# Performance work log

Hardware: AMD Instinct MI355X
Metric: run time of the kernel (lower is better)

The kernel has to match this reference:

```python
import jax, jax.numpy as jnp
import numpy as np

B, N, C, H = 2, 2048, 1024, 16
D = C // H
NEG = -1e9  # keras Softmax large negative for masked positions


def setup_inputs() -> dict:
    key = jax.random.key(0)
    ks = jax.random.split(key, 10)
    s = lambda fan_in: 1.0 / np.sqrt(fan_in)
    return {
        "x": jax.random.normal(ks[0], (B, N, C), jnp.float32),
        "mask": jnp.ones((B, 1, 1, N), jnp.bool_),
        "Wqkv": jax.random.normal(ks[1], (C, 3 * C), jnp.float32) * s(C),
        "bqkv": jnp.zeros((3 * C,), jnp.float32),
        "Wl": jax.random.normal(ks[2], (H, H), jnp.float32) * s(H),
        "bl": jnp.zeros((H,), jnp.float32),
        "Ww": jax.random.normal(ks[3], (H, H), jnp.float32) * s(H),
        "bw": jnp.zeros((H,), jnp.float32),
        "Wp": jax.random.normal(ks[4], (C, C), jnp.float32) * s(C),
        "bp": jnp.zeros((C,), jnp.float32),
    }


def reference(x, mask, Wqkv, bqkv, Wl, bl, Ww, bw, Wp, bp):
    scale = jnp.asarray(D ** -0.5, x.dtype)
    qkv = x @ Wqkv + bqkv                                  # [B,N,3C]
    qkv = qkv.reshape(B, N, 3, H, D).transpose(2, 0, 3, 1, 4)  # [3,B,H,N,D]
    q, k, v = qkv[0] * scale, qkv[1], qkv[2]
    attn = jnp.einsum("bhnd,bhmd->bhnm", q, k)             # [B,H,N,N]
    # pre-softmax talking-heads: mix head axis
    attn = jnp.einsum("bhnm,hg->bgnm", attn, Wl) + bl[None, :, None, None]
    # keras Softmax with boolean mask: add -1e9 where mask is False
    attn = attn + (1.0 - mask.astype(attn.dtype)) * NEG
    attn = jax.nn.softmax(attn, axis=-1)
    # post-softmax talking-heads
    attn = jnp.einsum("bhnm,hg->bgnm", attn, Ww) + bw[None, :, None, None]
    out = jnp.einsum("bhnm,bhmd->bhnd", attn, v)           # [B,H,N,D]
    out = out.transpose(0, 2, 1, 3).reshape(B, N, C)
    return out @ Wp + bp
```

## Files before the change

kernel.cpp:

```cpp
#include <hip/hip_runtime.h>
#include <hip/hip_bf16.h>


typedef __bf16 bf16_t;
typedef __bf16 bf16x8 __attribute__((ext_vector_type(8)));
typedef float f32x4 __attribute__((ext_vector_type(4)));

#define DEV static __device__ __forceinline__

static constexpr float NEGV = -1e9f;

DEV f32x4 mfma16(bf16x8 a, bf16x8 b, f32x4 c) {
  return __builtin_amdgcn_mfma_f32_16x16x32_bf16(a, b, c, 0, 0, 0);
}

DEV bf16x8 zero8() {
  bf16x8 z;
#pragma unroll
  for (int j = 0; j < 8; ++j) z[j] = (bf16_t)0.0f;
  return z;
}

DEV uint32_t pkbf(float lo, float hi) {
  union { bf16_t f; unsigned short s; } a, b;
  a.f = (bf16_t)lo; b.f = (bf16_t)hi;
  return (uint32_t)a.s | ((uint32_t)b.s << 16);
}

union U84 { uint32_t u[4]; bf16x8 v; };

__global__ __launch_bounds__(256) void mask_prep(const unsigned char* __restrict__ raw,
                                                 unsigned char* __restrict__ canon,
                                                 unsigned char* __restrict__ allflag) {
  __shared__ int c0, c12, f0, f1;
  const int tid = threadIdx.x;
  if (tid == 0) { c0 = 0; c12 = 0; f0 = 1; f1 = 1; }
  __syncthreads();
  int l0 = 0, l12 = 0;
  for (int i = tid; i < 4096; i += 256) {
    unsigned char v = raw[i];
    if (v) {
      int r = i & 3;
      if (r == 0) l0++;
      else if (r < 3) l12++;
    }
  }
  if (l0) atomicAdd(&c0, l0);
  if (l12) atomicAdd(&c12, l12);
  __syncthreads();
  const int mode = (c0 == 0) ? 2 : ((c12 > 0) ? 0 : 1);
  for (int i = tid; i < 4096; i += 256) {
    bool t;
    if (mode == 0)      t = raw[i] != 0;
    else if (mode == 1) t = ((const int*)raw)[i] != 0;
    else                t = ((const float*)raw)[i] != 0.0f;
    canon[i] = t ? 1 : 0;
    if (!t) atomicAnd(i < 2048 ? &f0 : &f1, 0);
  }
  __syncthreads();
  if (tid == 0) { allflag[0] = (unsigned char)f0; allflag[1] = (unsigned char)f1; }
}

__global__ __launch_bounds__(256) void gemm_kernel(
    const float* __restrict__ Af, const bf16_t* __restrict__ Ab,
    const float* __restrict__ Bw, const float* __restrict__ bias,
    float* __restrict__ outf,
    bf16_t* __restrict__ Qs, bf16_t* __restrict__ Ks, bf16_t* __restrict__ Vt,
    int K, int Nn, int epi) {
  __shared__ bf16_t As[64][40];
  __shared__ bf16_t Bs[64][40];
  const int tid = threadIdx.x;
  const int lane = tid & 63, wid = tid >> 6;
  const int bx = blockIdx.x, by = blockIdx.y;
  const int wr = (wid >> 1) * 32, wc = (wid & 1) * 32;
  const int lr = lane & 15, kq = lane >> 4;

  f32x4 acc[2][2];
#pragma unroll
  for (int i = 0; i < 2; ++i)
#pragma unroll
    for (int j = 0; j < 2; ++j) acc[i][j] = (f32x4){0.f, 0.f, 0.f, 0.f};

  for (int kt = 0; kt < K; kt += 32) {
    {
      const int row = tid >> 2, c8 = (tid & 3) * 8;
      if (epi == 0) {
        const float* p = Af + (size_t)(bx * 64 + row) * K + kt + c8;
        float4 v0 = *(const float4*)p;
        float4 v1 = *(const float4*)(p + 4);
        bf16x8 v;
        v[0] = (bf16_t)v0.x; v[1] = (bf16_t)v0.y; v[2] = (bf16_t)v0.z; v[3] = (bf16_t)v0.w;
        v[4] = (bf16_t)v1.x; v[5] = (bf16_t)v1.y; v[6] = (bf16_t)v1.z; v[7] = (bf16_t)v1.w;
        *(bf16x8*)&As[row][c8] = v;
      } else {
        *(bf16x8*)&As[row][c8] =
            *(const bf16x8*)(Ab + (size_t)(bx * 64 + row) * K + kt + c8);
      }
      const int krow = tid >> 3, n8 = (tid & 7) * 8;
      const float* bp = Bw + (size_t)(kt + krow) * Nn + by * 64 + n8;
      float4 b0 = *(const float4*)bp;
      float4 b1 = *(const float4*)(bp + 4);
      Bs[n8 + 0][krow] = (bf16_t)b0.x; Bs[n8 + 1][krow] = (bf16_t)b0.y;
      Bs[n8 + 2][krow] = (bf16_t)b0.z; Bs[n8 + 3][krow] = (bf16_t)b0.w;
      Bs[n8 + 4][krow] = (bf16_t)b1.x; Bs[n8 + 5][krow] = (bf16_t)b1.y;
      Bs[n8 + 6][krow] = (bf16_t)b1.z; Bs[n8 + 7][krow] = (bf16_t)b1.w;
    }
    __syncthreads();
#pragma unroll
    for (int rt = 0; rt < 2; ++rt) {
      bf16x8 af = *(const bf16x8*)&As[wr + rt * 16 + lr][kq * 8];
#pragma unroll
      for (int ct = 0; ct < 2; ++ct) {
        bf16x8 bf = *(const bf16x8*)&Bs[wc + ct * 16 + lr][kq * 8];
        acc[rt][ct] = mfma16(af, bf, acc[rt][ct]);
      }
    }
    __syncthreads();
  }

#pragma unroll
  for (int rt = 0; rt < 2; ++rt)
#pragma unroll
    for (int ct = 0; ct < 2; ++ct)
#pragma unroll
      for (int r = 0; r < 4; ++r) {
        const int grow = bx * 64 + wr + rt * 16 + kq * 4 + r;
        const int gcol = by * 64 + wc + ct * 16 + lr;
        const float v = acc[rt][ct][r] + bias[gcol];
        if (epi == 0) {
          const int t = gcol >> 10, h = (gcol >> 6) & 15, d = gcol & 63;
          const int b = grow >> 11, n = grow & 2047;
          if (t == 0)
            Qs[(((size_t)b * 16 + h) * 2048 + n) * 64 + d] = (bf16_t)(v * 0.125f);
          else if (t == 1)
            Ks[(((size_t)b * 16 + h) * 2048 + n) * 64 + d] = (bf16_t)v;
          else
            Vt[(((size_t)b * 16 + h) * 64 + d) * 2048 + n] = (bf16_t)v;
        } else {
          outf[(size_t)grow * Nn + gcol] = v;
        }
      }
}

__global__ __launch_bounds__(256) void vsum_kernel(const bf16_t* __restrict__ Vt,
                                                   float* __restrict__ Vsum) {
  const int lane = threadIdx.x & 63, wid = threadIdx.x >> 6;
  const int row = blockIdx.x * 4 + wid;
  const bf16_t* p = Vt + (size_t)row * 2048;
  float s = 0.f;
#pragma unroll
  for (int it = 0; it < 4; ++it) {
    bf16x8 v = *(const bf16x8*)(p + it * 512 + lane * 8);
#pragma unroll
    for (int j = 0; j < 8; ++j) s += (float)v[j];
  }
#pragma unroll
  for (int off = 32; off; off >>= 1) s += __shfl_xor(s, off);
  if (lane == 0) Vsum[row] = s;
}

__global__ __launch_bounds__(512, 2) void attn_fused(
    const bf16_t* __restrict__ Qs, const bf16_t* __restrict__ Ks,
    const bf16_t* __restrict__ Vt, const unsigned char* __restrict__ canon,
    const unsigned char* __restrict__ allflag,
    const float* __restrict__ Wl, const float* __restrict__ bl,
    const float* __restrict__ Ww, const float* __restrict__ bw,
    const float* __restrict__ Vsum, bf16_t* __restrict__ AO) {
  __shared__ uint32_t Sb[512 * 10];
  __shared__ uint32_t Fb[16 * 324];
  const int tid = threadIdx.x, lane = tid & 63, wid = tid >> 6;
  const int c = lane & 15, kq = lane >> 4;
  const int id = blockIdx.x;
  const int b = (id >> 2) & 1;
  const int nt = ((id >> 3) << 2) | (id & 3);
  const int n0 = nt * 16;
  const int bh0 = b * 16 + 2 * wid;
  const bool allt = allflag[b] != 0;

  bf16x8 wlf, wwf;
#pragma unroll
  for (int j = 0; j < 8; ++j) {
    const int k = kq * 8 + j;
    wlf[j] = (k < 16) ? (bf16_t)Wl[k * 16 + c] : (bf16_t)0.0f;
    wwf[j] = (k < 16) ? (bf16_t)Ww[k * 16 + c] : (bf16_t)0.0f;
  }
  f32x4 blv;
#pragma unroll
  for (int r = 0; r < 4; ++r) blv[r] = bl[kq * 4 + r];

  bf16x8 qf[2][2];
#pragma unroll
  for (int hh = 0; hh < 2; ++hh)
#pragma unroll
    for (int ks = 0; ks < 2; ++ks)
      qf[hh][ks] = *(const bf16x8*)(Qs + ((size_t)(bh0 + hh) * 2048 + n0 + c) * 64 +
                                    ks * 32 + kq * 8);

  struct KF { bf16x8 f[2][2][2]; };
  auto loadK = [&](int v) {
    KF k;
    const int m0 = (v < 64 ? v : 63) * 32;
#pragma unroll
    for (int hh = 0; hh < 2; ++hh)
#pragma unroll
      for (int mt = 0; mt < 2; ++mt)
#pragma unroll
        for (int ks = 0; ks < 2; ++ks)
          k.f[hh][mt][ks] = *(const bf16x8*)(Ks + ((size_t)(bh0 + hh) * 2048 + m0 +
                                                   mt * 16 + c) * 64 + ks * 32 + kq * 8);
    return k;
  };

  auto stage = [&](const KF& k) {
#pragma unroll
    for (int mt = 0; mt < 2; ++mt) {
      f32x4 a0 = (f32x4){0.f, 0.f, 0.f, 0.f};
      f32x4 a1 = (f32x4){0.f, 0.f, 0.f, 0.f};
      a0 = mfma16(qf[0][0], k.f[0][mt][0], a0);
      a0 = mfma16(qf[0][1], k.f[0][mt][1], a0);
      a1 = mfma16(qf[1][0], k.f[1][mt][0], a1);
      a1 = mfma16(qf[1][1], k.f[1][mt][1], a1);
#pragma unroll
      for (int r = 0; r < 4; ++r) {
        const int p = (kq * 4 + r) * 32 + mt * 16 + c;
        Sb[p * 10 + (wid ^ (kq & 1))] = pkbf(a0[r], a1[r]);
      }
    }
  };

  auto gatherS = [&](int pp) {
    const int prow = (wid * 4 + pp) * 16 + c;
    const int bp = (prow >> 7) & 1;
    if (kq < 2) {
      U84 t;
#pragma unroll
      for (int i = 0; i < 4; ++i) t.u[i] = Sb[prow * 10 + ((kq * 4 + i) ^ bp)];
      return t.v;
    }
    return zero8();
  };

  float lacc[4][2];
#pragma unroll
  for (int r = 0; r < 4; ++r) { lacc[r][0] = 0.f; lacc[r][1] = 0.f; }
  {
    KF kf = loadK(0);
    for (int u = 0; u < 64; ++u) {
      stage(kf);
      kf = loadK(u + 1);
      __syncthreads();
#pragma unroll
      for (int pp = 0; pp < 4; ++pp) {
        bf16x8 sf = gatherS(pp);
        f32x4 d1 = mfma16(wlf, sf, blv);
        if (!allt && !canon[b * 2048 + u * 32 + (pp & 1) * 16 + c]) {
          d1[0] += NEGV; d1[1] += NEGV; d1[2] += NEGV; d1[3] += NEGV;
        }
        const int ns = pp >> 1;
#pragma unroll
        for (int r = 0; r < 4; ++r) lacc[r][ns] += __expf(d1[r]);
      }
      __syncthreads();
    }
  }
  float invl[4][2];
#pragma unroll
  for (int r = 0; r < 4; ++r)
#pragma unroll
    for (int ns = 0; ns < 2; ++ns) {
      float s = lacc[r][ns];
      s += __shfl_xor(s, 1);
      s += __shfl_xor(s, 2);
      s += __shfl_xor(s, 4);
      s += __shfl_xor(s, 8);
      invl[r][ns] = 1.0f / s;
    }

  f32x4 oacc[2][4];
#pragma unroll
  for (int i = 0; i < 2; ++i)
#pragma unroll
    for (int j = 0; j < 4; ++j) oacc[i][j] = (f32x4){0.f, 0.f, 0.f, 0.f};
  {
    KF kf = loadK(0);
    for (int u = 0; u < 64; ++u) {
      stage(kf);
      kf = loadK(u + 1);
      __syncthreads();
      bf16x8 vr[2][4];
#pragma unroll
      for (int g2h = 0; g2h < 2; ++g2h)
#pragma unroll
        for (int dt = 0; dt < 4; ++dt)
          vr[g2h][dt] = *(const bf16x8*)(Vt + ((size_t)(bh0 + g2h) * 64 + dt * 16 + c) *
                                                  2048 + u * 32 + kq * 8);
#pragma unroll
      for (int pp = 0; pp < 4; ++pp) {
        bf16x8 sf = gatherS(pp);
        f32x4 d1 = mfma16(wlf, sf, blv);
        if (!allt && !canon[b * 2048 + u * 32 + (pp & 1) * 16 + c]) {
          d1[0] += NEGV; d1[1] += NEGV; d1[2] += NEGV; d1[3] += NEGV;
        }
        const int ns = pp >> 1;
        const float e0 = __expf(d1[0]) * invl[0][ns];
        const float e1 = __expf(d1[1]) * invl[1][ns];
        const float e2 = __expf(d1[2]) * invl[2][ns];
        const float e3 = __expf(d1[3]) * invl[3][ns];
        const int prow = (wid * 4 + pp) * 16 + c;
        uint2 ew;
        ew.x = pkbf(e0, e1);
        ew.y = pkbf(e2, e3);
        *(uint2*)&Sb[prow * 10 + kq * 2] = ew;
      }
      asm volatile("s_waitcnt lgkmcnt(0)" ::: "memory");
      __builtin_amdgcn_sched_barrier(0);
#pragma unroll
      for (int pp = 0; pp < 4; ++pp) {
        const int pg = wid * 4 + pp;
        const int prow = pg * 16 + c;
        bf16x8 ef;
        if (kq < 2) {
          U84 t;
#pragma unroll
          for (int i = 0; i < 4; ++i) t.u[i] = Sb[prow * 10 + kq * 4 + i];
          ef = t.v;
        } else ef = zero8();
        f32x4 d2 = mfma16(wwf, ef, (f32x4){0.f, 0.f, 0.f, 0.f});
        const int nl = pg >> 1, ml = (pg & 1) * 16 + c;
        const int wm = (ml >> 1) ^ ((nl & 3) << 2);
#pragma unroll
        for (int r = 0; r < 4; ++r)
          ((bf16_t*)Fb)[(((kq * 4 + r) * 324) + nl * 20 + wm) * 2 + (ml & 1)] =
              (bf16_t)d2[r];
      }
      __syncthreads();
#pragma unroll
      for (int g2h = 0; g2h < 2; ++g2h) {
        bf16x8 af = *(const bf16x8*)&Fb[(2 * wid + g2h) * 324 + c * 20 +
                                        ((kq ^ (c & 3)) << 2)];
#pragma unroll
        for (int dt = 0; dt < 4; ++dt)
          oacc[g2h][dt] = mfma16(af, vr[g2h][dt], oacc[g2h][dt]);
      }
    }
  }

#pragma unroll
  for (int g2h = 0; g2h < 2; ++g2h) {
    const int g2 = 2 * wid + g2h;
    const float bwv = bw[g2];
#pragma unroll
    for (int dt = 0; dt < 4; ++dt) {
      const float vs = Vsum[(size_t)(b * 16 + g2) * 64 + dt * 16 + c];
#pragma unroll
      for (int r = 0; r < 4; ++r) {
        const int n = n0 + kq * 4 + r;
        AO[((size_t)b * 2048 + n) * 1024 + g2 * 64 + dt * 16 + c] =
            (bf16_t)(oacc[g2h][dt][r] + bwv * vs);
      }
    }
  }
}

extern "C" void kernel_launch(void* const* d_in, const int* in_sizes, int n_in,
                              void* d_out, int out_size, void* d_ws, size_t ws_size,
                              hipStream_t stream) {
  const float* x = (const float*)d_in[0];
  const unsigned char* mask = (const unsigned char*)d_in[1];
  const float* Wqkv = (const float*)d_in[2];
  const float* bqkv = (const float*)d_in[3];
  const float* Wl = (const float*)d_in[4];
  const float* bl = (const float*)d_in[5];
  const float* Ww = (const float*)d_in[6];
  const float* bw = (const float*)d_in[7];
  const float* Wp = (const float*)d_in[8];
  const float* bp = (const float*)d_in[9];
  float* out = (float*)d_out;

  char* w = (char*)d_ws;
  auto alloc = [&](size_t bytes) {
    char* p = w;
    w += (bytes + 255) & ~(size_t)255;
    return p;
  };
  bf16_t* Qs = (bf16_t*)alloc((size_t)2 * 16 * 2048 * 64 * 2);
  bf16_t* Ks = (bf16_t*)alloc((size_t)2 * 16 * 2048 * 64 * 2);
  bf16_t* Vt = (bf16_t*)alloc((size_t)2 * 16 * 2048 * 64 * 2);
  bf16_t* AO = (bf16_t*)alloc((size_t)4096 * 1024 * 2);
  float* Vsum = (float*)alloc((size_t)2048 * 4);
  unsigned char* canon = (unsigned char*)alloc(4096);
  unsigned char* allflag = (unsigned char*)alloc(256);

  mask_prep<<<dim3(1), dim3(256), 0, stream>>>(mask, canon, allflag);
  gemm_kernel<<<dim3(64, 48), dim3(256), 0, stream>>>(
      x, (const bf16_t*)nullptr, Wqkv, bqkv, nullptr, Qs, Ks, Vt, 1024, 3072, 0);
  vsum_kernel<<<dim3(512), dim3(256), 0, stream>>>(Vt, Vsum);
  attn_fused<<<dim3(256), dim3(512), 0, stream>>>(Qs, Ks, Vt, canon, allflag, Wl, bl,
                                                  Ww, bw, Vsum, AO);
  gemm_kernel<<<dim3(64, 16), dim3(256), 0, stream>>>(
      (const float*)nullptr, AO, Wp, bp, out, nullptr, nullptr, nullptr, 1024, 1024, 1);
}
```

Measured before the change: 567.4 us.

## Double-buffer attention stages, halve block size, shuffle-based post-softmax mixing

Restructures the fused talking-heads attention kernel to use 256-thread blocks with each wave handling four heads. Double-buffered score and mixed-probability LDS tiles let the next tile's QK^T staging and the previous tile's PV MFMAs overlap the current tile's softmax work. This removes one barrier per iteration and the LDS round trip for the post-softmax head mix, which now goes through cross-lane shuffles. In exchange it uses more registers per wave (four heads of accumulators) and more LDS for the second buffers.

```diff
diff --git a/kernel.cpp b/kernel.cpp
--- a/kernel.cpp
+++ b/kernel.cpp
@@ -159,22 +159,21 @@
   if (lane == 0) Vsum[row] = s;
 }
 
-__global__ __launch_bounds__(512, 2) void attn_fused(
+__global__ __launch_bounds__(256, 2) void attn_fused(
     const bf16_t* __restrict__ Qs, const bf16_t* __restrict__ Ks,
     const bf16_t* __restrict__ Vt, const unsigned char* __restrict__ canon,
     const unsigned char* __restrict__ allflag,
     const float* __restrict__ Wl, const float* __restrict__ bl,
     const float* __restrict__ Ww, const float* __restrict__ bw,
     const float* __restrict__ Vsum, bf16_t* __restrict__ AO) {
-  __shared__ uint32_t Sb[512 * 10];
-  __shared__ uint32_t Fb[16 * 324];
+  __shared__ uint32_t Sb[2][5120];
+  __shared__ uint32_t Fb[2][16 * 260];
   const int tid = threadIdx.x, lane = tid & 63, wid = tid >> 6;
   const int c = lane & 15, kq = lane >> 4;
   const int id = blockIdx.x;
-  const int b = (id >> 2) & 1;
-  const int nt = ((id >> 3) << 2) | (id & 3);
-  const int n0 = nt * 16;
-  const int bh0 = b * 16 + 2 * wid;
+  const int b = id & 1;
+  const int n0 = (id >> 1) * 16;
+  const int h0 = 4 * wid;
   const bool allt = allflag[b] != 0;
 
   bf16x8 wlf, wwf;
@@ -188,86 +187,85 @@
 #pragma unroll
   for (int r = 0; r < 4; ++r) blv[r] = bl[kq * 4 + r];
 
-  bf16x8 qf[2][2];
-#pragma unroll
-  for (int hh = 0; hh < 2; ++hh)
+  bf16x8 qf[4][2];
+#pragma unroll
+  for (int hh = 0; hh < 4; ++hh)
 #pragma unroll
     for (int ks = 0; ks < 2; ++ks)
-      qf[hh][ks] = *(const bf16x8*)(Qs + ((size_t)(bh0 + hh) * 2048 + n0 + c) * 64 +
-                                    ks * 32 + kq * 8);
-
-  struct KF { bf16x8 f[2][2][2]; };
-  auto loadK = [&](int v) {
-    KF k;
-    const int m0 = (v < 64 ? v : 63) * 32;
-#pragma unroll
-    for (int hh = 0; hh < 2; ++hh)
-#pragma unroll
-      for (int mt = 0; mt < 2; ++mt)
-#pragma unroll
-        for (int ks = 0; ks < 2; ++ks)
-          k.f[hh][mt][ks] = *(const bf16x8*)(Ks + ((size_t)(bh0 + hh) * 2048 + m0 +
-                                                   mt * 16 + c) * 64 + ks * 32 + kq * 8);
-    return k;
+      qf[hh][ks] = *(const bf16x8*)(Qs + ((size_t)(b * 16 + h0 + hh) * 2048 + n0 + c) *
+                                             64 + ks * 32 + kq * 8);
+
+  auto stage = [&](int v, uint32_t* sb) {
+#pragma unroll
+    for (int hp = 0; hp < 2; ++hp) {
+      bf16x8 kf[2][2][2];
+#pragma unroll
+      for (int h2 = 0; h2 < 2; ++h2)
+#pragma unroll
+        for (int mt = 0; mt < 2; ++mt)
+#pragma unroll
+          for (int ks = 0; ks < 2; ++ks)
+            kf[h2][mt][ks] =
+                *(const bf16x8*)(Ks + ((size_t)(b * 16 + h0 + hp * 2 + h2) * 2048 +
+                                       v * 32 + mt * 16 + c) * 64 + ks * 32 + kq * 8);
+#pragma unroll
+      for (int mt = 0; mt < 2; ++mt) {
+        f32x4 a0 = (f32x4){0.f, 0.f, 0.f, 0.f};
+        f32x4 a1 = (f32x4){0.f, 0.f, 0.f, 0.f};
+        a0 = mfma16(qf[hp * 2 + 0][0], kf[0][mt][0], a0);
+        a0 = mfma16(qf[hp * 2 + 0][1], kf[0][mt][1], a0);
+        a1 = mfma16(qf[hp * 2 + 1][0], kf[1][mt][0], a1);
+        a1 = mfma16(qf[hp * 2 + 1][1], kf[1][mt][1], a1);
+#pragma unroll
+        for (int r = 0; r < 4; ++r) {
+          const int p = (kq * 4 + r) * 32 + mt * 16 + c;
+          sb[p * 10 + ((2 * wid + hp) ^ (kq & 1))] = pkbf(a0[r], a1[r]);
+        }
+      }
+    }
   };
 
-  auto stage = [&](const KF& k) {
-#pragma unroll
-    for (int mt = 0; mt < 2; ++mt) {
-      f32x4 a0 = (f32x4){0.f, 0.f, 0.f, 0.f};
-      f32x4 a1 = (f32x4){0.f, 0.f, 0.f, 0.f};
-      a0 = mfma16(qf[0][0], k.f[0][mt][0], a0);
-      a0 = mfma16(qf[0][1], k.f[0][mt][1], a0);
-      a1 = mfma16(qf[1][0], k.f[1][mt][0], a1);
-      a1 = mfma16(qf[1][1], k.f[1][mt][1], a1);
-#pragma unroll
-      for (int r = 0; r < 4; ++r) {
-        const int p = (kq * 4 + r) * 32 + mt * 16 + c;
-        Sb[p * 10 + (wid ^ (kq & 1))] = pkbf(a0[r], a1[r]);
-      }
-    }
-  };
-
-  auto gatherS = [&](int pp) {
-    const int prow = (wid * 4 + pp) * 16 + c;
+  auto gatherS = [&](const uint32_t* sb, int pp) {
+    const int prow = (wid * 8 + pp) * 16 + c;
     const int bp = (prow >> 7) & 1;
     if (kq < 2) {
       U84 t;
 #pragma unroll
-      for (int i = 0; i < 4; ++i) t.u[i] = Sb[prow * 10 + ((kq * 4 + i) ^ bp)];
+      for (int i = 0; i < 4; ++i) t.u[i] = sb[prow * 10 + ((kq * 4 + i) ^ bp)];
       return t.v;
     }
     return zero8();
   };
 
-  float lacc[4][2];
-#pragma unroll
-  for (int r = 0; r < 4; ++r) { lacc[r][0] = 0.f; lacc[r][1] = 0.f; }
-  {
-    KF kf = loadK(0);
-    for (int u = 0; u < 64; ++u) {
-      stage(kf);
-      kf = loadK(u + 1);
-      __syncthreads();
-#pragma unroll
-      for (int pp = 0; pp < 4; ++pp) {
-        bf16x8 sf = gatherS(pp);
-        f32x4 d1 = mfma16(wlf, sf, blv);
-        if (!allt && !canon[b * 2048 + u * 32 + (pp & 1) * 16 + c]) {
-          d1[0] += NEGV; d1[1] += NEGV; d1[2] += NEGV; d1[3] += NEGV;
-        }
-        const int ns = pp >> 1;
-#pragma unroll
-        for (int r = 0; r < 4; ++r) lacc[r][ns] += __expf(d1[r]);
-      }
-      __syncthreads();
-    }
-  }
-  float invl[4][2];
+  float lacc[4][4];
 #pragma unroll
   for (int r = 0; r < 4; ++r)
 #pragma unroll
-    for (int ns = 0; ns < 2; ++ns) {
+    for (int ns = 0; ns < 4; ++ns) lacc[r][ns] = 0.f;
+  stage(0, Sb[0]);
+  __syncthreads();
+  for (int u = 0; u < 64; ++u) {
+    const uint32_t* scur = Sb[u & 1];
+    uint32_t* snxt = Sb[(u + 1) & 1];
+#pragma unroll
+    for (int pp = 0; pp < 8; ++pp) {
+      bf16x8 sf = gatherS(scur, pp);
+      f32x4 d1 = mfma16(wlf, sf, blv);
+      if (!allt && !canon[b * 2048 + u * 32 + (pp & 1) * 16 + c]) {
+        d1[0] += NEGV; d1[1] += NEGV; d1[2] += NEGV; d1[3] += NEGV;
+      }
+      const int ns = pp >> 1;
+#pragma unroll
+      for (int r = 0; r < 4; ++r) lacc[r][ns] += __expf(d1[r]);
+    }
+    if (u < 63) stage(u + 1, snxt);
+    __syncthreads();
+  }
+  float invl[4][4];
+#pragma unroll
+  for (int r = 0; r < 4; ++r)
+#pragma unroll
+    for (int ns = 0; ns < 4; ++ns) {
       float s = lacc[r][ns];
       s += __shfl_xor(s, 1);
       s += __shfl_xor(s, 2);
@@ -276,78 +274,82 @@
       invl[r][ns] = 1.0f / s;
     }
 
-  f32x4 oacc[2][4];
-#pragma unroll
-  for (int i = 0; i < 2; ++i)
+  f32x4 oacc[4][4];
+#pragma unroll
+  for (int i = 0; i < 4; ++i)
 #pragma unroll
     for (int j = 0; j < 4; ++j) oacc[i][j] = (f32x4){0.f, 0.f, 0.f, 0.f};
+  stage(0, Sb[0]);
+  __syncthreads();
+  for (int u = 0; u < 64; ++u) {
+    const uint32_t* scur = Sb[u & 1];
+    uint32_t* snxt = Sb[(u + 1) & 1];
+    bf16_t* fcur = (bf16_t*)Fb[u & 1];
+    const uint32_t* fprev = Fb[(u + 1) & 1];
+    if (u > 0) {
+#pragma unroll
+      for (int hh = 0; hh < 4; ++hh) {
+        const int g2 = h0 + hh;
+        bf16x8 af = *(const bf16x8*)&fprev[g2 * 260 + c * 16 + ((kq ^ (c & 3)) << 2)];
+#pragma unroll
+        for (int dt = 0; dt < 4; ++dt) {
+          bf16x8 vf = *(const bf16x8*)(Vt + ((size_t)(b * 16 + g2) * 64 + dt * 16 + c) *
+                                                2048 + (u - 1) * 32 + kq * 8);
+          oacc[hh][dt] = mfma16(af, vf, oacc[hh][dt]);
+        }
+      }
+    }
+#pragma unroll
+    for (int pp = 0; pp < 8; ++pp) {
+      bf16x8 sf = gatherS(scur, pp);
+      f32x4 d1 = mfma16(wlf, sf, blv);
+      if (!allt && !canon[b * 2048 + u * 32 + (pp & 1) * 16 + c]) {
+        d1[0] += NEGV; d1[1] += NEGV; d1[2] += NEGV; d1[3] += NEGV;
+      }
+      const int ns = pp >> 1;
+      const float e0 = __expf(d1[0]) * invl[0][ns];
+      const float e1 = __expf(d1[1]) * invl[1][ns];
+      const float e2 = __expf(d1[2]) * invl[2][ns];
+      const float e3 = __expf(d1[3]) * invl[3][ns];
+      const uint32_t Aw = pkbf(e0, e1);
+      const uint32_t Bw2 = pkbf(e2, e3);
+      const int s0 = (c + 32 * kq) & 63;
+      const int s1 = (s0 + 16) & 63;
+      U84 ef;
+      ef.u[0] = (uint32_t)__shfl((int)Aw, s0);
+      ef.u[1] = (uint32_t)__shfl((int)Bw2, s0);
+      ef.u[2] = (uint32_t)__shfl((int)Aw, s1);
+      ef.u[3] = (uint32_t)__shfl((int)Bw2, s1);
+      bf16x8 efv = (kq < 2) ? ef.v : zero8();
+      f32x4 d2 = mfma16(wwf, efv, (f32x4){0.f, 0.f, 0.f, 0.f});
+      const int pg = wid * 8 + pp;
+      const int nl = pg >> 1, ml = (pg & 1) * 16 + c;
+      const int wm = (ml >> 1) ^ ((nl & 3) << 2);
+#pragma unroll
+      for (int r = 0; r < 4; ++r)
+        fcur[(kq * 4 + r) * 520 + nl * 32 + wm * 2 + (ml & 1)] = (bf16_t)d2[r];
+    }
+    if (u < 63) stage(u + 1, snxt);
+    __syncthreads();
+  }
   {
-    KF kf = loadK(0);
-    for (int u = 0; u < 64; ++u) {
-      stage(kf);
-      kf = loadK(u + 1);
-      __syncthreads();
-      bf16x8 vr[2][4];
-#pragma unroll
-      for (int g2h = 0; g2h < 2; ++g2h)
-#pragma unroll
-        for (int dt = 0; dt < 4; ++dt)
-          vr[g2h][dt] = *(const bf16x8*)(Vt + ((size_t)(bh0 + g2h) * 64 + dt * 16 + c) *
-                                                  2048 + u * 32 + kq * 8);
-#pragma unroll
-      for (int pp = 0; pp < 4; ++pp) {
-        bf16x8 sf = gatherS(pp);
-        f32x4 d1 = mfma16(wlf, sf, blv);
-        if (!allt && !canon[b * 2048 + u * 32 + (pp & 1) * 16 + c]) {
-          d1[0] += NEGV; d1[1] += NEGV; d1[2] += NEGV; d1[3] += NEGV;
-        }
-        const int ns = pp >> 1;
-        const float e0 = __expf(d1[0]) * invl[0][ns];
-        const float e1 = __expf(d1[1]) * invl[1][ns];
-        const float e2 = __expf(d1[2]) * invl[2][ns];
-        const float e3 = __expf(d1[3]) * invl[3][ns];
-        const int prow = (wid * 4 + pp) * 16 + c;
-        uint2 ew;
-        ew.x = pkbf(e0, e1);
-        ew.y = pkbf(e2, e3);
-        *(uint2*)&Sb[prow * 10 + kq * 2] = ew;
-      }
-      asm volatile("s_waitcnt lgkmcnt(0)" ::: "memory");
-      __builtin_amdgcn_sched_barrier(0);
-#pragma unroll
-      for (int pp = 0; pp < 4; ++pp) {
-        const int pg = wid * 4 + pp;
-        const int prow = pg * 16 + c;
-        bf16x8 ef;
-        if (kq < 2) {
-          U84 t;
-#pragma unroll
-          for (int i = 0; i < 4; ++i) t.u[i] = Sb[prow * 10 + kq * 4 + i];
-          ef = t.v;
-        } else ef = zero8();
-        f32x4 d2 = mfma16(wwf, ef, (f32x4){0.f, 0.f, 0.f, 0.f});
-        const int nl = pg >> 1, ml = (pg & 1) * 16 + c;
-        const int wm = (ml >> 1) ^ ((nl & 3) << 2);
-#pragma unroll
-        for (int r = 0; r < 4; ++r)
-          ((bf16_t*)Fb)[(((kq * 4 + r) * 324) + nl * 20 + wm) * 2 + (ml & 1)] =
-              (bf16_t)d2[r];
-      }
-      __syncthreads();
-#pragma unroll
-      for (int g2h = 0; g2h < 2; ++g2h) {
-        bf16x8 af = *(const bf16x8*)&Fb[(2 * wid + g2h) * 324 + c * 20 +
-                                        ((kq ^ (c & 3)) << 2)];
-#pragma unroll
-        for (int dt = 0; dt < 4; ++dt)
-          oacc[g2h][dt] = mfma16(af, vr[g2h][dt], oacc[g2h][dt]);
-      }
-    }
-  }
-
-#pragma unroll
-  for (int g2h = 0; g2h < 2; ++g2h) {
-    const int g2 = 2 * wid + g2h;
+    const uint32_t* fprev = Fb[1];
+#pragma unroll
+    for (int hh = 0; hh < 4; ++hh) {
+      const int g2 = h0 + hh;
+      bf16x8 af = *(const bf16x8*)&fprev[g2 * 260 + c * 16 + ((kq ^ (c & 3)) << 2)];
+#pragma unroll
+      for (int dt = 0; dt < 4; ++dt) {
+        bf16x8 vf = *(const bf16x8*)(Vt + ((size_t)(b * 16 + g2) * 64 + dt * 16 + c) *
+                                              2048 + 63 * 32 + kq * 8);
+        oacc[hh][dt] = mfma16(af, vf, oacc[hh][dt]);
+      }
+    }
+  }
+
+#pragma unroll
+  for (int hh = 0; hh < 4; ++hh) {
+    const int g2 = h0 + hh;
     const float bwv = bw[g2];
 #pragma unroll
     for (int dt = 0; dt < 4; ++dt) {
@@ -356,7 +358,7 @@
       for (int r = 0; r < 4; ++r) {
         const int n = n0 + kq * 4 + r;
         AO[((size_t)b * 2048 + n) * 1024 + g2 * 64 + dt * 16 + c] =
-            (bf16_t)(oacc[g2h][dt][r] + bwv * vs);
+            (bf16_t)(oacc[hh][dt][r] + bwv * vs);
       }
     }
   }
@@ -395,7 +397,7 @@
   gemm_kernel<<<dim3(64, 48), dim3(256), 0, stream>>>(
       x, (const bf16_t*)nullptr, Wqkv, bqkv, nullptr, Qs, Ks, Vt, 1024, 3072, 0);
   vsum_kernel<<<dim3(512), dim3(256), 0, stream>>>(Vt, Vsum);
-  attn_fused<<<dim3(256), dim3(512), 0, stream>>>(Qs, Ks, Vt, canon, allflag, Wl, bl,
+  attn_fused<<<dim3(256), dim3(256), 0, stream>>>(Qs, Ks, Vt, canon, allflag, Wl, bl,
                                                   Ww, bw, Vsum, AO);
   gemm_kernel<<<dim3(64, 16), dim3(256), 0, stream>>>(
       (const float*)nullptr, AO, Wp, bp, out, nullptr, nullptr, nullptr, 1024, 1024, 1);
```

Result: slower. 720.0 us (+26.9%).
